# Performance work log

Measured on AMD Instinct MI355X. Metric: run time of the kernel, lower is better.

## Reference

```python
import jax, jax.numpy as jnp
import numpy as np

N_HEAD = 16

def _proj1x1(W, b, x):
    # kernel-size-1 Conv1d == channel-wise linear: x (B, C_in, T) -> (B, C_out, T)
    return jnp.einsum('oc,bct->bot', W, x) + b[None, :, None]

def setup_inputs() -> dict:
    key = jax.random.key(0)
    B, C, T = 2, 512, 2048
    ks = jax.random.split(key, 11)
    s = 0.02
    return {
        'q': jax.random.normal(ks[0], (B, C, T), jnp.float32),
        'k': jax.random.normal(ks[1], (B, C, T), jnp.float32),
        'v': jax.random.normal(ks[2], (B, C, T), jnp.float32),
        'mask': jnp.ones((B, 1, T), dtype=bool),
        'Wq': jax.random.normal(ks[3], (C, C), jnp.float32) * s,
        'bq': jax.random.normal(ks[4], (C,), jnp.float32) * s,
        'Wk': jax.random.normal(ks[5], (C, C), jnp.float32) * s,
        'bk': jax.random.normal(ks[6], (C,), jnp.float32) * s,
        'Wv': jax.random.normal(ks[7], (C, C), jnp.float32) * s,
        'bv': jax.random.normal(ks[8], (C,), jnp.float32) * s,
        'Wp': jax.random.normal(ks[9], (C, C), jnp.float32) * s,
        'bp': jax.random.normal(ks[10], (C,), jnp.float32) * s,
    }

def reference(q, k, v, mask, Wq, bq, Wk, bk, Wv, bv, Wp, bp):
    B, C, T = q.shape
    H = N_HEAD
    D = C // H
    scale = 1.0 / np.sqrt(D).astype(np.float32)
    # 1x1 conv projections, then split heads: (B,C,T) -> (B,H,T,D)
    qh = _proj1x1(Wq, bq, q).reshape(B, H, D, T).swapaxes(2, 3)
    kh = _proj1x1(Wk, bk, k).reshape(B, H, D, T).swapaxes(2, 3)
    vh = _proj1x1(Wv, bv, v).reshape(B, H, D, T).swapaxes(2, 3)
    # scores (B,H,Tq,Tk) with key-side mask
    att = jnp.einsum('bhqd,bhkd->bhqk', qh * scale, kh)
    att = jnp.where(mask[:, :, None, :], att, -jnp.inf)
    att = jax.nn.softmax(att, axis=-1)
    # value masking (as in original: v * mask before AV matmul)
    vm = vh * mask[:, :, :, None].astype(vh.dtype)
    out = jnp.einsum('bhqk,bhkd->bhqd', att, vm)
    out = out.swapaxes(2, 3).reshape(B, C, T)
    out = _proj1x1(Wp, bp, out) * mask.astype(out.dtype)
    return (out, mask)
```

## Files before the change

### kernel.cpp

```cpp
#include <hip/hip_runtime.h>

using u16 = unsigned short;
typedef float  f32x4 __attribute__((ext_vector_type(4)));
typedef __bf16 bf8_t __attribute__((ext_vector_type(8)));
typedef u16    u16x4 __attribute__((ext_vector_type(4)));
typedef unsigned int u32x2 __attribute__((ext_vector_type(2)));

#define NB 2
#define NH 16
#define NT 2048
#define ND 32
#define NC 512
#define QK_SCALE 0.17677669529663687f
#define LOG2E    1.4426950408889634f

__device__ __forceinline__ u16 f2bf(float f) {
  unsigned int u = __float_as_uint(f);
  u += 0x7fffu + ((u >> 16) & 1u);
  return (u16)(u >> 16);
}

__device__ __forceinline__ unsigned int cvt_pk_bf16(float a, float b) {
  unsigned int r;
  asm("v_cvt_pk_bf16_f32 %0, %1, %2" : "=v"(r) : "v"(a), "v"(b));
  return r;
}

__device__ __forceinline__ f32x4 mfma16(bf8_t a, bf8_t b, f32x4 c) {
  return __builtin_amdgcn_mfma_f32_16x16x32_bf16(a, b, c, 0, 0, 0);
}

__global__ __launch_bounds__(256) void convert_kernel(
    const float* __restrict__ Wq, const float* __restrict__ Wk,
    const float* __restrict__ Wv, const float* __restrict__ Wp,
    const void* __restrict__ mraw,
    u16* __restrict__ Wc, float* __restrict__ maskf, float* __restrict__ maskb,
    float* __restrict__ outtail) {
  int bid = blockIdx.x;
  if (bid < 1024) {
    int idx = (bid * 256 + (int)threadIdx.x) * 4;
    int m   = idx >> 18;
    int off = idx & 262143;
    const float* W = (m == 0) ? Wq : (m == 1) ? Wk : (m == 2) ? Wv : Wp;
    float s = (m == 0) ? (QK_SCALE * LOG2E) : 1.0f;
    f32x4 wv = *(const f32x4*)(W + off);
    u16x4 pk;
    #pragma unroll
    for (int r = 0; r < 4; ++r) pk[r] = f2bf(wv[r] * s);
    *(u16x4*)(Wc + (size_t)m * (NC * NC) + off) = pk;
  } else {
    unsigned int w0 = *(const unsigned int*)mraw;
    bool intlay = (w0 == 1u);
    #pragma unroll
    for (int kk = 0; kk < 16; ++kk) {
      int j = (int)threadIdx.x + kk * 256;
      float mv;
      if (intlay) mv = ((const int*)mraw)[j] ? 1.0f : 0.0f;
      else        mv = ((const unsigned char*)mraw)[j] ? 1.0f : 0.0f;
      maskf[j]   = mv;
      maskb[j]   = (mv - 1.0f) * 1e30f;
      outtail[j] = mv;
    }
  }
}

__global__ __launch_bounds__(256) void transpose_kernel(
    const float* __restrict__ q, const float* __restrict__ k,
    const float* __restrict__ v, u16* __restrict__ Xt) {
  __shared__ float tile[32][33];
  int z = blockIdx.z;
  int m = z >> 1, b = z & 1;
  const float* src = (m == 0) ? q : (m == 1) ? k : v;
  int t0 = blockIdx.x * 32, c0 = blockIdx.y * 32;
  int tx = threadIdx.x, ty = threadIdx.y;
  #pragma unroll
  for (int j = 0; j < 4; ++j)
    tile[ty + j * 8][tx] = src[(size_t)(b * NC + c0 + ty + j * 8) * NT + t0 + tx];
  __syncthreads();
  u16* dst = Xt + (size_t)m * (NB * NT * NC);
  #pragma unroll
  for (int j = 0; j < 4; ++j)
    dst[((size_t)b * NT + t0 + ty + j * 8) * NC + c0 + tx] = f2bf(tile[tx][ty + j * 8]);
}

__global__ __launch_bounds__(256) void proj_kernel(
    const u16* __restrict__ Wc, const u16* __restrict__ Xt,
    const float* __restrict__ bq, const float* __restrict__ bk, const float* __restrict__ bv,
    u16* __restrict__ Qw, u16* __restrict__ Kw, u16* __restrict__ Vw,
    const float* __restrict__ maskf) {
  int z = blockIdx.z;
  const u16* W = Wc + (size_t)z * (NC * NC);
  const float* bias = (z == 0) ? bq : (z == 1) ? bk : bv;
  int tid = threadIdx.x, wid = tid >> 6, lane = tid & 63;
  int lq = lane & 15, g = lane >> 4;
  int om0 = blockIdx.x * 64;
  int b   = blockIdx.y >> 4;
  int t0  = (blockIdx.y & 15) * 128 + wid * 32;
  const u16* Xb = Xt + (size_t)z * (NB * NT * NC) + (size_t)b * NT * NC;

  const f32x4 zero = {0.f, 0.f, 0.f, 0.f};
  f32x4 acc[4][2];
  #pragma unroll
  for (int mt = 0; mt < 4; ++mt)
    #pragma unroll
    for (int nt = 0; nt < 2; ++nt) acc[mt][nt] = zero;

  for (int ks = 0; ks < 16; ++ks) {
    bf8_t af[4], bfr[2];
    #pragma unroll
    for (int mt = 0; mt < 4; ++mt)
      af[mt] = *(const bf8_t*)(W + (size_t)(om0 + mt * 16 + lq) * NC + ks * 32 + 8 * g);
    #pragma unroll
    for (int nt = 0; nt < 2; ++nt)
      bfr[nt] = *(const bf8_t*)(Xb + (size_t)(t0 + nt * 16 + lq) * NC + ks * 32 + 8 * g);
    #pragma unroll
    for (int mt = 0; mt < 4; ++mt)
      #pragma unroll
      for (int nt = 0; nt < 2; ++nt)
        acc[mt][nt] = mfma16(af[mt], bfr[nt], acc[mt][nt]);
  }

  float sc = (z == 0) ? (QK_SCALE * LOG2E) : 1.0f;
  #pragma unroll
  for (int mt = 0; mt < 4; ++mt) {
    int ob = om0 + mt * 16 + 4 * g;
    float b4[4];
    #pragma unroll
    for (int r = 0; r < 4; ++r) b4[r] = bias[ob + r] * sc;
    #pragma unroll
    for (int nt = 0; nt < 2; ++nt) {
      int t = t0 + nt * 16 + lq;
      if (z < 2) {
        u16x4 pk;
        #pragma unroll
        for (int r = 0; r < 4; ++r) pk[r] = f2bf(acc[mt][nt][r] + b4[r]);
        u16* dst = (z == 0) ? Qw : Kw;
        *(u16x4*)(dst + ((size_t)(b * NH + (ob >> 5)) * NT + t) * ND + (ob & 31)) = pk;
      } else {
        float mv = maskf[b * NT + t];
        #pragma unroll
        for (int r = 0; r < 4; ++r)
          Vw[(size_t)(b * NC + ob + r) * NT + t] = f2bf((acc[mt][nt][r] + b4[r]) * mv);
      }
    }
  }
}

__global__ __launch_bounds__(256) void attn_kernel(
    const u16* __restrict__ Qw, const u16* __restrict__ Kw, const u16* __restrict__ Vw,
    u16* __restrict__ Ow, const float* __restrict__ maskb) {
  __shared__ u16 plds[4][32][128];
  int tid = threadIdx.x, wid = tid >> 6, lane = tid & 63;
  int lq = lane & 15, g = lane >> 4;
  int bh = blockIdx.y, b = bh >> 4, h = bh & 15;
  int q0 = blockIdx.x * 128 + wid * 32;
  const u16* Qb = Qw + (size_t)bh * NT * ND;
  const u16* Kb = Kw + (size_t)bh * NT * ND;
  const u16* Vb = Vw + (size_t)(b * NC + h * ND) * NT;
  const float* mbp = maskb + b * NT;
  char* pbase = (char*)&plds[wid][0][0];

  bf8_t ones;
  #pragma unroll
  for (int j = 0; j < 8; ++j) ones[j] = (__bf16)1.0f;

  bf8_t qf[2];
  #pragma unroll
  for (int c = 0; c < 2; ++c)
    qf[c] = *(const bf8_t*)(Qb + (size_t)(q0 + c * 16 + lq) * ND + 8 * g);

  const f32x4 zero = {0.f, 0.f, 0.f, 0.f};
  f32x4 acc[3][2];
  #pragma unroll
  for (int dt = 0; dt < 3; ++dt)
    #pragma unroll
    for (int c = 0; c < 2; ++c) acc[dt][c] = zero;
  float mrun[2] = {0.f, 0.f};

  for (int kt = 0; kt < 16; ++kt) {
    int tkb = kt * 128;
    f32x4 st[8][2];
    #pragma unroll
    for (int rt = 0; rt < 8; ++rt) {
      f32x4 bias = *(const f32x4*)(mbp + tkb + rt * 16 + 4 * g);
      bf8_t kf = *(const bf8_t*)(Kb + (size_t)(tkb + rt * 16 + lq) * ND + 8 * g);
      st[rt][0] = mfma16(kf, qf[0], bias);
      st[rt][1] = mfma16(kf, qf[1], bias);
    }
    bf8_t vf[2][4];
    #pragma unroll
    for (int dt = 0; dt < 2; ++dt)
      #pragma unroll
      for (int kk = 0; kk < 4; ++kk)
        vf[dt][kk] = *(const bf8_t*)(Vb + (size_t)(dt * 16 + lq) * NT + tkb + kk * 32 + 8 * g);

    #pragma unroll
    for (int c = 0; c < 2; ++c) {
      float tm = -1e30f;
      #pragma unroll
      for (int rt = 0; rt < 8; ++rt) {
        tm = fmaxf(fmaxf(st[rt][c][0], st[rt][c][1]), tm);
        tm = fmaxf(fmaxf(st[rt][c][2], st[rt][c][3]), tm);
      }
      tm = fmaxf(tm, __shfl_xor(tm, 16));
      tm = fmaxf(tm, __shfl_xor(tm, 32));
      if (__any(tm > mrun[c] + 8.0f)) {
        float mnew = fmaxf(mrun[c], tm);
        float al = __builtin_amdgcn_exp2f(mrun[c] - mnew);
        mrun[c] = mnew;
        acc[0][c] *= al; acc[1][c] *= al; acc[2][c] *= al;
      }
      float nm = -mrun[c];
      int row = c * 16 + lq;
      #pragma unroll
      for (int rt = 0; rt < 8; ++rt) {
        float p0 = __builtin_amdgcn_exp2f(st[rt][c][0] + nm);
        float p1 = __builtin_amdgcn_exp2f(st[rt][c][1] + nm);
        float p2 = __builtin_amdgcn_exp2f(st[rt][c][2] + nm);
        float p3 = __builtin_amdgcn_exp2f(st[rt][c][3] + nm);
        u32x2 w;
        w[0] = cvt_pk_bf16(p0, p1);
        w[1] = cvt_pk_bf16(p2, p3);
        *(u32x2*)(pbase + row * 256 + ((rt * 32 + 8 * g) ^ ((row & 7) << 4))) = w;
      }
    }
    #pragma unroll
    for (int kk = 0; kk < 4; ++kk) {
      bf8_t pf[2];
      #pragma unroll
      for (int c = 0; c < 2; ++c) {
        int row = c * 16 + lq;
        pf[c] = *(const bf8_t*)(pbase + row * 256 + ((kk * 64 + 16 * g) ^ ((row & 7) << 4)));
      }
      #pragma unroll
      for (int c = 0; c < 2; ++c) {
        acc[0][c] = mfma16(vf[0][kk], pf[c], acc[0][c]);
        acc[1][c] = mfma16(vf[1][kk], pf[c], acc[1][c]);
        acc[2][c] = mfma16(ones,      pf[c], acc[2][c]);
      }
    }
  }
  #pragma unroll
  for (int c = 0; c < 2; ++c) {
    float inv = 1.0f / acc[2][c][0];
    int t = q0 + c * 16 + lq;
    #pragma unroll
    for (int dt = 0; dt < 2; ++dt) {
      u32x2 o;
      o[0] = cvt_pk_bf16(acc[dt][c][0] * inv, acc[dt][c][1] * inv);
      o[1] = cvt_pk_bf16(acc[dt][c][2] * inv, acc[dt][c][3] * inv);
      *(u32x2*)(Ow + ((size_t)bh * NT + t) * ND + dt * 16 + 4 * g) = o;
    }
  }
}

__global__ __launch_bounds__(256) void outproj_kernel(
    const u16* __restrict__ Wc, const u16* __restrict__ Ow,
    const float* __restrict__ bp, float* __restrict__ out,
    const float* __restrict__ maskf) {
  const u16* W = Wc + (size_t)3 * NC * NC;
  int tid = threadIdx.x, wid = tid >> 6, lane = tid & 63;
  int lq = lane & 15, g = lane >> 4;
  int om0 = blockIdx.x * 64;
  int b   = blockIdx.y >> 4;
  int t0  = (blockIdx.y & 15) * 128 + wid * 32;
  const u16* Ob = Ow + (size_t)b * NH * NT * ND;

  const f32x4 zero = {0.f, 0.f, 0.f, 0.f};
  f32x4 acc[4][2];
  #pragma unroll
  for (int mt = 0; mt < 4; ++mt)
    #pragma unroll
    for (int nt = 0; nt < 2; ++nt) acc[mt][nt] = zero;

  for (int ks = 0; ks < 16; ++ks) {
    bf8_t af[4], bfr[2];
    #pragma unroll
    for (int mt = 0; mt < 4; ++mt)
      af[mt] = *(const bf8_t*)(W + (size_t)(om0 + mt * 16 + lq) * NC + ks * 32 + 8 * g);
    #pragma unroll
    for (int nt = 0; nt < 2; ++nt)
      bfr[nt] = *(const bf8_t*)(Ob + ((size_t)ks * NT + t0 + nt * 16 + lq) * ND + 8 * g);
    #pragma unroll
    for (int mt = 0; mt < 4; ++mt)
      #pragma unroll
      for (int nt = 0; nt < 2; ++nt)
        acc[mt][nt] = mfma16(af[mt], bfr[nt], acc[mt][nt]);
  }
  #pragma unroll
  for (int mt = 0; mt < 4; ++mt) {
    int ob = om0 + mt * 16 + 4 * g;
    float b4[4];
    #pragma unroll
    for (int r = 0; r < 4; ++r) b4[r] = bp[ob + r];
    #pragma unroll
    for (int nt = 0; nt < 2; ++nt) {
      int t = t0 + nt * 16 + lq;
      float mv = maskf[b * NT + t];
      #pragma unroll
      for (int r = 0; r < 4; ++r)
        out[(size_t)(b * NC + ob + r) * NT + t] = (acc[mt][nt][r] + b4[r]) * mv;
    }
  }
}

extern "C" void kernel_launch(void* const* d_in, const int* in_sizes, int n_in,
                              void* d_out, int out_size, void* d_ws, size_t ws_size,
                              hipStream_t stream) {
  const float* q  = (const float*)d_in[0];
  const float* k  = (const float*)d_in[1];
  const float* v  = (const float*)d_in[2];
  const void*  mr = d_in[3];
  const float* Wq = (const float*)d_in[4];
  const float* bq = (const float*)d_in[5];
  const float* Wk = (const float*)d_in[6];
  const float* bk = (const float*)d_in[7];
  const float* Wv = (const float*)d_in[8];
  const float* bv = (const float*)d_in[9];
  const float* Wp = (const float*)d_in[10];
  const float* bp = (const float*)d_in[11];
  float* out = (float*)d_out;

  u16* Wc = (u16*)d_ws;
  u16* Xt = Wc + (size_t)4 * NC * NC;
  u16* Qw = Xt + (size_t)3 * NB * NT * NC;
  u16* Kw = Qw + (size_t)NB * NT * NC;
  u16* Vw = Kw + (size_t)NB * NT * NC;
  u16* Ow = Vw + (size_t)NB * NT * NC;
  float* maskf   = (float*)(Ow + (size_t)NB * NT * NC);
  float* maskb   = maskf + (size_t)NB * NT;
  float* outtail = out + (size_t)NB * NC * NT;

  convert_kernel<<<1025, 256, 0, stream>>>(Wq, Wk, Wv, Wp, mr, Wc, maskf, maskb, outtail);
  transpose_kernel<<<dim3(NT / 32, NC / 32, 6), dim3(32, 8), 0, stream>>>(q, k, v, Xt);
  proj_kernel<<<dim3(8, 32, 3), 256, 0, stream>>>(Wc, Xt, bq, bk, bv, Qw, Kw, Vw, maskf);
  attn_kernel<<<dim3(16, 32), 256, 0, stream>>>(Qw, Kw, Vw, Ow, maskb);
  outproj_kernel<<<dim3(8, 32), 256, 0, stream>>>(Wc, Ow, bp, out, maskf);
}
```

Before: 203.9 us.

## Shrink per-block tiles to raise grid size and add register prefetch in GEMMs

Halves the output tile per block in the projection, attention and output-projection kernels, doubling or quadrupling the number of blocks so more CUs are busy on this small problem. The GEMM loops now software-prefetch the next k-slice into registers while issuing MFMAs. Attention handles 16 query rows per wave instead of 32 and lowers the lazy-rescale threshold. The trade is less data reuse per wave, more redundant K/V and weight loads, and more launch overhead from extra blocks.

```diff
diff --git a/kernel.cpp b/kernel.cpp
--- a/kernel.cpp
+++ b/kernel.cpp
@@ -83,7 +83,7 @@
     dst[((size_t)b * NT + t0 + ty + j * 8) * NC + c0 + tx] = f2bf(tile[tx][ty + j * 8]);
 }
 
-__global__ __launch_bounds__(256) void proj_kernel(
+__global__ __launch_bounds__(256, 4) void proj_kernel(
     const u16* __restrict__ Wc, const u16* __restrict__ Xt,
     const float* __restrict__ bq, const float* __restrict__ bk, const float* __restrict__ bv,
     u16* __restrict__ Qw, u16* __restrict__ Kw, u16* __restrict__ Vw,
@@ -93,36 +93,36 @@
   const float* bias = (z == 0) ? bq : (z == 1) ? bk : bv;
   int tid = threadIdx.x, wid = tid >> 6, lane = tid & 63;
   int lq = lane & 15, g = lane >> 4;
-  int om0 = blockIdx.x * 64;
+  int om0 = blockIdx.x * 32;
   int b   = blockIdx.y >> 4;
   int t0  = (blockIdx.y & 15) * 128 + wid * 32;
   const u16* Xb = Xt + (size_t)z * (NB * NT * NC) + (size_t)b * NT * NC;
 
+  const u16* Wr0 = W  + (size_t)(om0 + lq) * NC + 8 * g;
+  const u16* Wr1 = W  + (size_t)(om0 + 16 + lq) * NC + 8 * g;
+  const u16* Xr0 = Xb + (size_t)(t0 + lq) * NC + 8 * g;
+  const u16* Xr1 = Xb + (size_t)(t0 + 16 + lq) * NC + 8 * g;
+
   const f32x4 zero = {0.f, 0.f, 0.f, 0.f};
-  f32x4 acc[4][2];
-  #pragma unroll
-  for (int mt = 0; mt < 4; ++mt)
-    #pragma unroll
-    for (int nt = 0; nt < 2; ++nt) acc[mt][nt] = zero;
-
+  f32x4 acc[2][2];
+  acc[0][0] = zero; acc[0][1] = zero; acc[1][0] = zero; acc[1][1] = zero;
+
+  bf8_t a0 = *(const bf8_t*)Wr0, a1 = *(const bf8_t*)Wr1;
+  bf8_t x0 = *(const bf8_t*)Xr0, x1 = *(const bf8_t*)Xr1;
   for (int ks = 0; ks < 16; ++ks) {
-    bf8_t af[4], bfr[2];
-    #pragma unroll
-    for (int mt = 0; mt < 4; ++mt)
-      af[mt] = *(const bf8_t*)(W + (size_t)(om0 + mt * 16 + lq) * NC + ks * 32 + 8 * g);
-    #pragma unroll
-    for (int nt = 0; nt < 2; ++nt)
-      bfr[nt] = *(const bf8_t*)(Xb + (size_t)(t0 + nt * 16 + lq) * NC + ks * 32 + 8 * g);
-    #pragma unroll
-    for (int mt = 0; mt < 4; ++mt)
-      #pragma unroll
-      for (int nt = 0; nt < 2; ++nt)
-        acc[mt][nt] = mfma16(af[mt], bfr[nt], acc[mt][nt]);
+    int kn = (ks < 15 ? ks + 1 : ks) * 32;
+    bf8_t an0 = *(const bf8_t*)(Wr0 + kn), an1 = *(const bf8_t*)(Wr1 + kn);
+    bf8_t xn0 = *(const bf8_t*)(Xr0 + kn), xn1 = *(const bf8_t*)(Xr1 + kn);
+    acc[0][0] = mfma16(a0, x0, acc[0][0]);
+    acc[0][1] = mfma16(a0, x1, acc[0][1]);
+    acc[1][0] = mfma16(a1, x0, acc[1][0]);
+    acc[1][1] = mfma16(a1, x1, acc[1][1]);
+    a0 = an0; a1 = an1; x0 = xn0; x1 = xn1;
   }
 
   float sc = (z == 0) ? (QK_SCALE * LOG2E) : 1.0f;
   #pragma unroll
-  for (int mt = 0; mt < 4; ++mt) {
+  for (int mt = 0; mt < 2; ++mt) {
     int ob = om0 + mt * 16 + 4 * g;
     float b4[4];
     #pragma unroll
@@ -146,14 +146,14 @@
   }
 }
 
-__global__ __launch_bounds__(256) void attn_kernel(
+__global__ __launch_bounds__(256, 4) void attn_kernel(
     const u16* __restrict__ Qw, const u16* __restrict__ Kw, const u16* __restrict__ Vw,
     u16* __restrict__ Ow, const float* __restrict__ maskb) {
-  __shared__ u16 plds[4][32][128];
+  __shared__ u16 plds[4][16][128];
   int tid = threadIdx.x, wid = tid >> 6, lane = tid & 63;
   int lq = lane & 15, g = lane >> 4;
   int bh = blockIdx.y, b = bh >> 4, h = bh & 15;
-  int q0 = blockIdx.x * 128 + wid * 32;
+  int q0 = blockIdx.x * 64 + wid * 16;
   const u16* Qb = Qw + (size_t)bh * NT * ND;
   const u16* Kb = Kw + (size_t)bh * NT * ND;
   const u16* Vb = Vw + (size_t)(b * NC + h * ND) * NT;
@@ -164,28 +164,21 @@
   #pragma unroll
   for (int j = 0; j < 8; ++j) ones[j] = (__bf16)1.0f;
 
-  bf8_t qf[2];
-  #pragma unroll
-  for (int c = 0; c < 2; ++c)
-    qf[c] = *(const bf8_t*)(Qb + (size_t)(q0 + c * 16 + lq) * ND + 8 * g);
+  bf8_t qf = *(const bf8_t*)(Qb + (size_t)(q0 + lq) * ND + 8 * g);
 
   const f32x4 zero = {0.f, 0.f, 0.f, 0.f};
-  f32x4 acc[3][2];
-  #pragma unroll
-  for (int dt = 0; dt < 3; ++dt)
-    #pragma unroll
-    for (int c = 0; c < 2; ++c) acc[dt][c] = zero;
-  float mrun[2] = {0.f, 0.f};
+  f32x4 acc[3];
+  acc[0] = zero; acc[1] = zero; acc[2] = zero;
+  float mrun = 0.f;
 
   for (int kt = 0; kt < 16; ++kt) {
     int tkb = kt * 128;
-    f32x4 st[8][2];
+    f32x4 st[8];
     #pragma unroll
     for (int rt = 0; rt < 8; ++rt) {
       f32x4 bias = *(const f32x4*)(mbp + tkb + rt * 16 + 4 * g);
       bf8_t kf = *(const bf8_t*)(Kb + (size_t)(tkb + rt * 16 + lq) * ND + 8 * g);
-      st[rt][0] = mfma16(kf, qf[0], bias);
-      st[rt][1] = mfma16(kf, qf[1], bias);
+      st[rt] = mfma16(kf, qf, bias);
     }
     bf8_t vf[2][4];
     #pragma unroll
@@ -194,113 +187,89 @@
       for (int kk = 0; kk < 4; ++kk)
         vf[dt][kk] = *(const bf8_t*)(Vb + (size_t)(dt * 16 + lq) * NT + tkb + kk * 32 + 8 * g);
 
-    #pragma unroll
-    for (int c = 0; c < 2; ++c) {
-      float tm = -1e30f;
-      #pragma unroll
-      for (int rt = 0; rt < 8; ++rt) {
-        tm = fmaxf(fmaxf(st[rt][c][0], st[rt][c][1]), tm);
-        tm = fmaxf(fmaxf(st[rt][c][2], st[rt][c][3]), tm);
-      }
-      tm = fmaxf(tm, __shfl_xor(tm, 16));
-      tm = fmaxf(tm, __shfl_xor(tm, 32));
-      if (__any(tm > mrun[c] + 8.0f)) {
-        float mnew = fmaxf(mrun[c], tm);
-        float al = __builtin_amdgcn_exp2f(mrun[c] - mnew);
-        mrun[c] = mnew;
-        acc[0][c] *= al; acc[1][c] *= al; acc[2][c] *= al;
-      }
-      float nm = -mrun[c];
-      int row = c * 16 + lq;
-      #pragma unroll
-      for (int rt = 0; rt < 8; ++rt) {
-        float p0 = __builtin_amdgcn_exp2f(st[rt][c][0] + nm);
-        float p1 = __builtin_amdgcn_exp2f(st[rt][c][1] + nm);
-        float p2 = __builtin_amdgcn_exp2f(st[rt][c][2] + nm);
-        float p3 = __builtin_amdgcn_exp2f(st[rt][c][3] + nm);
-        u32x2 w;
-        w[0] = cvt_pk_bf16(p0, p1);
-        w[1] = cvt_pk_bf16(p2, p3);
-        *(u32x2*)(pbase + row * 256 + ((rt * 32 + 8 * g) ^ ((row & 7) << 4))) = w;
-      }
+    float tm = -1e30f;
+    #pragma unroll
+    for (int rt = 0; rt < 8; ++rt) {
+      tm = fmaxf(fmaxf(st[rt][0], st[rt][1]), tm);
+      tm = fmaxf(fmaxf(st[rt][2], st[rt][3]), tm);
+    }
+    tm = fmaxf(tm, __shfl_xor(tm, 16));
+    tm = fmaxf(tm, __shfl_xor(tm, 32));
+    if (__any(tm > mrun + 2.0f)) {
+      float mnew = fmaxf(mrun, tm);
+      float al = __builtin_amdgcn_exp2f(mrun - mnew);
+      mrun = mnew;
+      acc[0] *= al; acc[1] *= al; acc[2] *= al;
+    }
+    float nm = -mrun;
+    #pragma unroll
+    for (int rt = 0; rt < 8; ++rt) {
+      float p0 = __builtin_amdgcn_exp2f(st[rt][0] + nm);
+      float p1 = __builtin_amdgcn_exp2f(st[rt][1] + nm);
+      float p2 = __builtin_amdgcn_exp2f(st[rt][2] + nm);
+      float p3 = __builtin_amdgcn_exp2f(st[rt][3] + nm);
+      u32x2 w;
+      w[0] = cvt_pk_bf16(p0, p1);
+      w[1] = cvt_pk_bf16(p2, p3);
+      *(u32x2*)(pbase + lq * 256 + ((rt * 32 + 8 * g) ^ ((lq & 7) << 4))) = w;
     }
     #pragma unroll
     for (int kk = 0; kk < 4; ++kk) {
-      bf8_t pf[2];
-      #pragma unroll
-      for (int c = 0; c < 2; ++c) {
-        int row = c * 16 + lq;
-        pf[c] = *(const bf8_t*)(pbase + row * 256 + ((kk * 64 + 16 * g) ^ ((row & 7) << 4)));
-      }
-      #pragma unroll
-      for (int c = 0; c < 2; ++c) {
-        acc[0][c] = mfma16(vf[0][kk], pf[c], acc[0][c]);
-        acc[1][c] = mfma16(vf[1][kk], pf[c], acc[1][c]);
-        acc[2][c] = mfma16(ones,      pf[c], acc[2][c]);
-      }
-    }
-  }
-  #pragma unroll
-  for (int c = 0; c < 2; ++c) {
-    float inv = 1.0f / acc[2][c][0];
-    int t = q0 + c * 16 + lq;
-    #pragma unroll
-    for (int dt = 0; dt < 2; ++dt) {
-      u32x2 o;
-      o[0] = cvt_pk_bf16(acc[dt][c][0] * inv, acc[dt][c][1] * inv);
-      o[1] = cvt_pk_bf16(acc[dt][c][2] * inv, acc[dt][c][3] * inv);
-      *(u32x2*)(Ow + ((size_t)bh * NT + t) * ND + dt * 16 + 4 * g) = o;
-    }
-  }
-}
-
-__global__ __launch_bounds__(256) void outproj_kernel(
+      bf8_t pf = *(const bf8_t*)(pbase + lq * 256 + ((kk * 64 + 16 * g) ^ ((lq & 7) << 4)));
+      acc[0] = mfma16(vf[0][kk], pf, acc[0]);
+      acc[1] = mfma16(vf[1][kk], pf, acc[1]);
+      acc[2] = mfma16(ones,      pf, acc[2]);
+    }
+  }
+  float inv = 1.0f / acc[2][0];
+  int t = q0 + lq;
+  #pragma unroll
+  for (int dt = 0; dt < 2; ++dt) {
+    u32x2 o;
+    o[0] = cvt_pk_bf16(acc[dt][0] * inv, acc[dt][1] * inv);
+    o[1] = cvt_pk_bf16(acc[dt][2] * inv, acc[dt][3] * inv);
+    *(u32x2*)(Ow + ((size_t)bh * NT + t) * ND + dt * 16 + 4 * g) = o;
+  }
+}
+
+__global__ __launch_bounds__(256, 4) void outproj_kernel(
     const u16* __restrict__ Wc, const u16* __restrict__ Ow,
     const float* __restrict__ bp, float* __restrict__ out,
     const float* __restrict__ maskf) {
   const u16* W = Wc + (size_t)3 * NC * NC;
   int tid = threadIdx.x, wid = tid >> 6, lane = tid & 63;
   int lq = lane & 15, g = lane >> 4;
-  int om0 = blockIdx.x * 64;
-  int b   = blockIdx.y >> 4;
-  int t0  = (blockIdx.y & 15) * 128 + wid * 32;
+  int om0 = blockIdx.x * 32;
+  int b   = blockIdx.y >> 5;
+  int t0  = (blockIdx.y & 31) * 64 + wid * 16;
   const u16* Ob = Ow + (size_t)b * NH * NT * ND;
 
+  const u16* Wr0 = W + (size_t)(om0 + lq) * NC + 8 * g;
+  const u16* Wr1 = W + (size_t)(om0 + 16 + lq) * NC + 8 * g;
+
   const f32x4 zero = {0.f, 0.f, 0.f, 0.f};
-  f32x4 acc[4][2];
-  #pragma unroll
-  for (int mt = 0; mt < 4; ++mt)
-    #pragma unroll
-    for (int nt = 0; nt < 2; ++nt) acc[mt][nt] = zero;
-
+  f32x4 acc0 = zero, acc1 = zero;
+
+  bf8_t a0 = *(const bf8_t*)Wr0, a1 = *(const bf8_t*)Wr1;
+  bf8_t x0 = *(const bf8_t*)(Ob + (size_t)(t0 + lq) * ND + 8 * g);
   for (int ks = 0; ks < 16; ++ks) {
-    bf8_t af[4], bfr[2];
-    #pragma unroll
-    for (int mt = 0; mt < 4; ++mt)
-      af[mt] = *(const bf8_t*)(W + (size_t)(om0 + mt * 16 + lq) * NC + ks * 32 + 8 * g);
-    #pragma unroll
-    for (int nt = 0; nt < 2; ++nt)
-      bfr[nt] = *(const bf8_t*)(Ob + ((size_t)ks * NT + t0 + nt * 16 + lq) * ND + 8 * g);
-    #pragma unroll
-    for (int mt = 0; mt < 4; ++mt)
-      #pragma unroll
-      for (int nt = 0; nt < 2; ++nt)
-        acc[mt][nt] = mfma16(af[mt], bfr[nt], acc[mt][nt]);
-  }
-  #pragma unroll
-  for (int mt = 0; mt < 4; ++mt) {
+    int kn = (ks < 15) ? ks + 1 : ks;
+    bf8_t an0 = *(const bf8_t*)(Wr0 + kn * 32);
+    bf8_t an1 = *(const bf8_t*)(Wr1 + kn * 32);
+    bf8_t xn0 = *(const bf8_t*)(Ob + ((size_t)kn * NT + t0 + lq) * ND + 8 * g);
+    acc0 = mfma16(a0, x0, acc0);
+    acc1 = mfma16(a1, x0, acc1);
+    a0 = an0; a1 = an1; x0 = xn0;
+  }
+  int t = t0 + lq;
+  float mv = maskf[b * NT + t];
+  #pragma unroll
+  for (int mt = 0; mt < 2; ++mt) {
     int ob = om0 + mt * 16 + 4 * g;
-    float b4[4];
-    #pragma unroll
-    for (int r = 0; r < 4; ++r) b4[r] = bp[ob + r];
-    #pragma unroll
-    for (int nt = 0; nt < 2; ++nt) {
-      int t = t0 + nt * 16 + lq;
-      float mv = maskf[b * NT + t];
-      #pragma unroll
-      for (int r = 0; r < 4; ++r)
-        out[(size_t)(b * NC + ob + r) * NT + t] = (acc[mt][nt][r] + b4[r]) * mv;
-    }
+    const f32x4& a = mt ? acc1 : acc0;
+    #pragma unroll
+    for (int r = 0; r < 4; ++r)
+      out[(size_t)(b * NC + ob + r) * NT + t] = (a[r] + bp[ob + r]) * mv;
   }
 }
 
@@ -333,7 +302,7 @@
 
   convert_kernel<<<1025, 256, 0, stream>>>(Wq, Wk, Wv, Wp, mr, Wc, maskf, maskb, outtail);
   transpose_kernel<<<dim3(NT / 32, NC / 32, 6), dim3(32, 8), 0, stream>>>(q, k, v, Xt);
-  proj_kernel<<<dim3(8, 32, 3), 256, 0, stream>>>(Wc, Xt, bq, bk, bv, Qw, Kw, Vw, maskf);
-  attn_kernel<<<dim3(16, 32), 256, 0, stream>>>(Qw, Kw, Vw, Ow, maskb);
-  outproj_kernel<<<dim3(8, 32), 256, 0, stream>>>(Wc, Ow, bp, out, maskf);
-}
+  proj_kernel<<<dim3(16, 32, 3), 256, 0, stream>>>(Wc, Xt, bq, bk, bv, Qw, Kw, Vw, maskf);
+  attn_kernel<<<dim3(32, 32), 256, 0, stream>>>(Qw, Kw, Vw, Ow, maskb);
+  outproj_kernel<<<dim3(16, 64), 256, 0, stream>>>(Wc, Ow, bp, out, maskf);
+}
```

New measurement: 265.7 us. 30.3% more time.

## Split attention over key halves and merge partials inside output projection

Applied to the files above, without the earlier changes.

The attention kernel now splits the key sequence into two halves across a new grid dimension, which doubles the block count to fill more compute units. Each half writes unnormalized fp32 partial outputs plus its running max and sum. The output projection kernel merges the two partials with log-sum-exp rescaling before its MFMA, and uses smaller tiles for more blocks. The cost is extra fp32 partial traffic to global memory and merge arithmetic in the projection. The rescale threshold is also lowered from 8 to 2, and launch bounds are added.

```diff
diff --git a/kernel.cpp b/kernel.cpp
--- a/kernel.cpp
+++ b/kernel.cpp
@@ -146,13 +146,14 @@
   }
 }
 
-__global__ __launch_bounds__(256) void attn_kernel(
+__global__ __launch_bounds__(256, 4) void attn_kernel(
     const u16* __restrict__ Qw, const u16* __restrict__ Kw, const u16* __restrict__ Vw,
-    u16* __restrict__ Ow, const float* __restrict__ maskb) {
+    float* __restrict__ Op, float* __restrict__ ml, const float* __restrict__ maskb) {
   __shared__ u16 plds[4][32][128];
   int tid = threadIdx.x, wid = tid >> 6, lane = tid & 63;
   int lq = lane & 15, g = lane >> 4;
   int bh = blockIdx.y, b = bh >> 4, h = bh & 15;
+  int z  = blockIdx.z;
   int q0 = blockIdx.x * 128 + wid * 32;
   const u16* Qb = Qw + (size_t)bh * NT * ND;
   const u16* Kb = Kw + (size_t)bh * NT * ND;
@@ -177,7 +178,7 @@
     for (int c = 0; c < 2; ++c) acc[dt][c] = zero;
   float mrun[2] = {0.f, 0.f};
 
-  for (int kt = 0; kt < 16; ++kt) {
+  for (int kt = z * 8; kt < z * 8 + 8; ++kt) {
     int tkb = kt * 128;
     f32x4 st[8][2];
     #pragma unroll
@@ -204,7 +205,7 @@
       }
       tm = fmaxf(tm, __shfl_xor(tm, 16));
       tm = fmaxf(tm, __shfl_xor(tm, 32));
-      if (__any(tm > mrun[c] + 8.0f)) {
+      if (__any(tm > mrun[c] + 2.0f)) {
         float mnew = fmaxf(mrun[c], tm);
         float al = __builtin_amdgcn_exp2f(mrun[c] - mnew);
         mrun[c] = mnew;
@@ -240,67 +241,74 @@
       }
     }
   }
+  size_t pofs = (size_t)z * NB * NH * NT * ND;
+  size_t mofs = (size_t)z * NB * NH * NT;
   #pragma unroll
   for (int c = 0; c < 2; ++c) {
-    float inv = 1.0f / acc[2][c][0];
     int t = q0 + c * 16 + lq;
-    #pragma unroll
-    for (int dt = 0; dt < 2; ++dt) {
-      u32x2 o;
-      o[0] = cvt_pk_bf16(acc[dt][c][0] * inv, acc[dt][c][1] * inv);
-      o[1] = cvt_pk_bf16(acc[dt][c][2] * inv, acc[dt][c][3] * inv);
-      *(u32x2*)(Ow + ((size_t)bh * NT + t) * ND + dt * 16 + 4 * g) = o;
-    }
-  }
-}
-
-__global__ __launch_bounds__(256) void outproj_kernel(
-    const u16* __restrict__ Wc, const u16* __restrict__ Ow,
+    if (g == 0) {
+      float2 mlv; mlv.x = mrun[c]; mlv.y = acc[2][c][0];
+      *(float2*)(ml + (mofs + (size_t)bh * NT + t) * 2) = mlv;
+    }
+    #pragma unroll
+    for (int dt = 0; dt < 2; ++dt)
+      *(f32x4*)(Op + pofs + ((size_t)bh * NT + t) * ND + dt * 16 + 4 * g) = acc[dt][c];
+  }
+}
+
+__global__ __launch_bounds__(256, 4) void outproj_kernel(
+    const u16* __restrict__ Wc, const float* __restrict__ Op,
+    const float* __restrict__ ml,
     const float* __restrict__ bp, float* __restrict__ out,
     const float* __restrict__ maskf) {
   const u16* W = Wc + (size_t)3 * NC * NC;
   int tid = threadIdx.x, wid = tid >> 6, lane = tid & 63;
   int lq = lane & 15, g = lane >> 4;
-  int om0 = blockIdx.x * 64;
-  int b   = blockIdx.y >> 4;
-  int t0  = (blockIdx.y & 15) * 128 + wid * 32;
-  const u16* Ob = Ow + (size_t)b * NH * NT * ND;
+  int om0 = blockIdx.x * 32;
+  int b   = blockIdx.y >> 5;
+  int t0  = (blockIdx.y & 31) * 64 + wid * 16;
+  int t   = t0 + lq;
+
+  const u16* Wr0 = W + (size_t)(om0 + lq) * NC + 8 * g;
+  const u16* Wr1 = W + (size_t)(om0 + 16 + lq) * NC + 8 * g;
+  const size_t PS = (size_t)NB * NH * NT * ND;
+  const size_t MS = (size_t)NB * NH * NT;
 
   const f32x4 zero = {0.f, 0.f, 0.f, 0.f};
-  f32x4 acc[4][2];
-  #pragma unroll
-  for (int mt = 0; mt < 4; ++mt)
-    #pragma unroll
-    for (int nt = 0; nt < 2; ++nt) acc[mt][nt] = zero;
+  f32x4 acc0 = zero, acc1 = zero;
 
   for (int ks = 0; ks < 16; ++ks) {
-    bf8_t af[4], bfr[2];
-    #pragma unroll
-    for (int mt = 0; mt < 4; ++mt)
-      af[mt] = *(const bf8_t*)(W + (size_t)(om0 + mt * 16 + lq) * NC + ks * 32 + 8 * g);
-    #pragma unroll
-    for (int nt = 0; nt < 2; ++nt)
-      bfr[nt] = *(const bf8_t*)(Ob + ((size_t)ks * NT + t0 + nt * 16 + lq) * ND + 8 * g);
-    #pragma unroll
-    for (int mt = 0; mt < 4; ++mt)
-      #pragma unroll
-      for (int nt = 0; nt < 2; ++nt)
-        acc[mt][nt] = mfma16(af[mt], bfr[nt], acc[mt][nt]);
-  }
-  #pragma unroll
-  for (int mt = 0; mt < 4; ++mt) {
+    bf8_t a0 = *(const bf8_t*)(Wr0 + ks * 32);
+    bf8_t a1 = *(const bf8_t*)(Wr1 + ks * 32);
+    size_t qb = (size_t)(b * NH + ks) * NT + t;
+    float2 v1 = *(const float2*)(ml + qb * 2);
+    float2 v2 = *(const float2*)(ml + (MS + qb) * 2);
+    size_t ob = qb * ND + 8 * g;
+    f32x4 o1a = *(const f32x4*)(Op + ob);
+    f32x4 o1b = *(const f32x4*)(Op + ob + 4);
+    f32x4 o2a = *(const f32x4*)(Op + PS + ob);
+    f32x4 o2b = *(const f32x4*)(Op + PS + ob + 4);
+    float m  = fmaxf(v1.x, v2.x);
+    float e1 = __builtin_amdgcn_exp2f(v1.x - m);
+    float e2 = __builtin_amdgcn_exp2f(v2.x - m);
+    float inv = 1.0f / (v1.y * e1 + v2.y * e2);
+    float c1 = e1 * inv, c2 = e2 * inv;
+    union { bf8_t v; unsigned int u[4]; } xf;
+    xf.u[0] = cvt_pk_bf16(o1a[0] * c1 + o2a[0] * c2, o1a[1] * c1 + o2a[1] * c2);
+    xf.u[1] = cvt_pk_bf16(o1a[2] * c1 + o2a[2] * c2, o1a[3] * c1 + o2a[3] * c2);
+    xf.u[2] = cvt_pk_bf16(o1b[0] * c1 + o2b[0] * c2, o1b[1] * c1 + o2b[1] * c2);
+    xf.u[3] = cvt_pk_bf16(o1b[2] * c1 + o2b[2] * c2, o1b[3] * c1 + o2b[3] * c2);
+    acc0 = mfma16(a0, xf.v, acc0);
+    acc1 = mfma16(a1, xf.v, acc1);
+  }
+  float mv = maskf[b * NT + t];
+  #pragma unroll
+  for (int mt = 0; mt < 2; ++mt) {
     int ob = om0 + mt * 16 + 4 * g;
-    float b4[4];
-    #pragma unroll
-    for (int r = 0; r < 4; ++r) b4[r] = bp[ob + r];
-    #pragma unroll
-    for (int nt = 0; nt < 2; ++nt) {
-      int t = t0 + nt * 16 + lq;
-      float mv = maskf[b * NT + t];
-      #pragma unroll
-      for (int r = 0; r < 4; ++r)
-        out[(size_t)(b * NC + ob + r) * NT + t] = (acc[mt][nt][r] + b4[r]) * mv;
-    }
+    const f32x4& a = mt ? acc1 : acc0;
+    #pragma unroll
+    for (int r = 0; r < 4; ++r)
+      out[(size_t)(b * NC + ob + r) * NT + t] = (a[r] + bp[ob + r]) * mv;
   }
 }
 
@@ -326,14 +334,15 @@
   u16* Qw = Xt + (size_t)3 * NB * NT * NC;
   u16* Kw = Qw + (size_t)NB * NT * NC;
   u16* Vw = Kw + (size_t)NB * NT * NC;
-  u16* Ow = Vw + (size_t)NB * NT * NC;
-  float* maskf   = (float*)(Ow + (size_t)NB * NT * NC);
-  float* maskb   = maskf + (size_t)NB * NT;
+  float* Op    = (float*)(Vw + (size_t)NB * NT * NC);
+  float* ml    = Op + (size_t)2 * NB * NH * NT * ND;
+  float* maskf = ml + (size_t)2 * NB * NH * NT * 2;
+  float* maskb = maskf + (size_t)NB * NT;
   float* outtail = out + (size_t)NB * NC * NT;
 
   convert_kernel<<<1025, 256, 0, stream>>>(Wq, Wk, Wv, Wp, mr, Wc, maskf, maskb, outtail);
   transpose_kernel<<<dim3(NT / 32, NC / 32, 6), dim3(32, 8), 0, stream>>>(q, k, v, Xt);
   proj_kernel<<<dim3(8, 32, 3), 256, 0, stream>>>(Wc, Xt, bq, bk, bv, Qw, Kw, Vw, maskf);
-  attn_kernel<<<dim3(16, 32), 256, 0, stream>>>(Qw, Kw, Vw, Ow, maskb);
-  outproj_kernel<<<dim3(8, 32), 256, 0, stream>>>(Wc, Ow, bp, out, maskf);
-}
+  attn_kernel<<<dim3(16, 32, 2), 256, 0, stream>>>(Qw, Kw, Vw, Op, ml, maskb);
+  outproj_kernel<<<dim3(16, 64), 256, 0, stream>>>(Wc, Op, ml, bp, out, maskf);
+}
```

New measurement: 271.1 us. 1.33x slower.

## Split attention KV range across wave pairs and fuse prep kernels

Applied to the files above, without the earlier changes.

The attention kernel now gives each block 64 queries and splits the 16 KV tiles between two wave pairs. The partial accumulators, running maxima and sums are merged through shared memory at the end, and the grid doubles to 1024 blocks for better occupancy and latency hiding. The weight/mask conversion and the input transpose are merged into one launch to remove a kernel launch. The rescale threshold drops from 8 to 2, and launch bounds request 4 blocks per SM. The costs are extra syncs, an LDS merge step and duplicated Q loads.

```diff
diff --git a/kernel.cpp b/kernel.cpp
--- a/kernel.cpp
+++ b/kernel.cpp
@@ -30,15 +30,20 @@
   return __builtin_amdgcn_mfma_f32_16x16x32_bf16(a, b, c, 0, 0, 0);
 }
 
-__global__ __launch_bounds__(256) void convert_kernel(
+__global__ __launch_bounds__(256) void prep_kernel(
+    const float* __restrict__ q, const float* __restrict__ k,
+    const float* __restrict__ v, u16* __restrict__ Xt,
     const float* __restrict__ Wq, const float* __restrict__ Wk,
     const float* __restrict__ Wv, const float* __restrict__ Wp,
     const void* __restrict__ mraw,
     u16* __restrict__ Wc, float* __restrict__ maskf, float* __restrict__ maskb,
     float* __restrict__ outtail) {
-  int bid = blockIdx.x;
-  if (bid < 1024) {
-    int idx = (bid * 256 + (int)threadIdx.x) * 4;
+  int z = blockIdx.z;
+  int tx = threadIdx.x, ty = threadIdx.y;
+  if (z == 6) {
+    int bid = blockIdx.y * 64 + blockIdx.x;
+    int tid = ty * 32 + tx;
+    int idx = (bid * 256 + tid) * 4;
     int m   = idx >> 18;
     int off = idx & 262143;
     const float* W = (m == 0) ? Wq : (m == 1) ? Wk : (m == 2) ? Wv : Wp;
@@ -48,31 +53,26 @@
     #pragma unroll
     for (int r = 0; r < 4; ++r) pk[r] = f2bf(wv[r] * s);
     *(u16x4*)(Wc + (size_t)m * (NC * NC) + off) = pk;
-  } else {
-    unsigned int w0 = *(const unsigned int*)mraw;
-    bool intlay = (w0 == 1u);
-    #pragma unroll
-    for (int kk = 0; kk < 16; ++kk) {
-      int j = (int)threadIdx.x + kk * 256;
-      float mv;
-      if (intlay) mv = ((const int*)mraw)[j] ? 1.0f : 0.0f;
-      else        mv = ((const unsigned char*)mraw)[j] ? 1.0f : 0.0f;
-      maskf[j]   = mv;
-      maskb[j]   = (mv - 1.0f) * 1e30f;
-      outtail[j] = mv;
-    }
-  }
-}
-
-__global__ __launch_bounds__(256) void transpose_kernel(
-    const float* __restrict__ q, const float* __restrict__ k,
-    const float* __restrict__ v, u16* __restrict__ Xt) {
+    if (bid == 0) {
+      unsigned int w0 = *(const unsigned int*)mraw;
+      bool intlay = (w0 == 1u);
+      #pragma unroll
+      for (int kk = 0; kk < 16; ++kk) {
+        int j = tid + kk * 256;
+        float mv;
+        if (intlay) mv = ((const int*)mraw)[j] ? 1.0f : 0.0f;
+        else        mv = ((const unsigned char*)mraw)[j] ? 1.0f : 0.0f;
+        maskf[j]   = mv;
+        maskb[j]   = (mv - 1.0f) * 1e30f;
+        outtail[j] = mv;
+      }
+    }
+    return;
+  }
   __shared__ float tile[32][33];
-  int z = blockIdx.z;
   int m = z >> 1, b = z & 1;
   const float* src = (m == 0) ? q : (m == 1) ? k : v;
   int t0 = blockIdx.x * 32, c0 = blockIdx.y * 32;
-  int tx = threadIdx.x, ty = threadIdx.y;
   #pragma unroll
   for (int j = 0; j < 4; ++j)
     tile[ty + j * 8][tx] = src[(size_t)(b * NC + c0 + ty + j * 8) * NT + t0 + tx];
@@ -146,14 +146,15 @@
   }
 }
 
-__global__ __launch_bounds__(256) void attn_kernel(
+__global__ __launch_bounds__(256, 4) void attn_kernel(
     const u16* __restrict__ Qw, const u16* __restrict__ Kw, const u16* __restrict__ Vw,
     u16* __restrict__ Ow, const float* __restrict__ maskb) {
   __shared__ u16 plds[4][32][128];
   int tid = threadIdx.x, wid = tid >> 6, lane = tid & 63;
   int lq = lane & 15, g = lane >> 4;
   int bh = blockIdx.y, b = bh >> 4, h = bh & 15;
-  int q0 = blockIdx.x * 128 + wid * 32;
+  int kvz = wid >> 1;
+  int q0  = blockIdx.x * 64 + (wid & 1) * 32;
   const u16* Qb = Qw + (size_t)bh * NT * ND;
   const u16* Kb = Kw + (size_t)bh * NT * ND;
   const u16* Vb = Vw + (size_t)(b * NC + h * ND) * NT;
@@ -177,7 +178,7 @@
     for (int c = 0; c < 2; ++c) acc[dt][c] = zero;
   float mrun[2] = {0.f, 0.f};
 
-  for (int kt = 0; kt < 16; ++kt) {
+  for (int kt = kvz * 8; kt < kvz * 8 + 8; ++kt) {
     int tkb = kt * 128;
     f32x4 st[8][2];
     #pragma unroll
@@ -204,7 +205,7 @@
       }
       tm = fmaxf(tm, __shfl_xor(tm, 16));
       tm = fmaxf(tm, __shfl_xor(tm, 32));
-      if (__any(tm > mrun[c] + 8.0f)) {
+      if (__any(tm > mrun[c] + 2.0f)) {
         float mnew = fmaxf(mrun[c], tm);
         float al = __builtin_amdgcn_exp2f(mrun[c] - mnew);
         mrun[c] = mnew;
@@ -240,16 +241,49 @@
       }
     }
   }
-  #pragma unroll
-  for (int c = 0; c < 2; ++c) {
-    float inv = 1.0f / acc[2][c][0];
-    int t = q0 + c * 16 + lq;
-    #pragma unroll
-    for (int dt = 0; dt < 2; ++dt) {
-      u32x2 o;
-      o[0] = cvt_pk_bf16(acc[dt][c][0] * inv, acc[dt][c][1] * inv);
-      o[1] = cvt_pk_bf16(acc[dt][c][2] * inv, acc[dt][c][3] * inv);
-      *(u32x2*)(Ow + ((size_t)bh * NT + t) * ND + dt * 16 + 4 * g) = o;
+
+  __syncthreads();
+  float* cb = (float*)plds;
+  if (wid >= 2) {
+    int p = wid - 2;
+    char* cbO = (char*)(cb + p * 1024);
+    float* cbML = cb + 2048 + p * 64;
+    #pragma unroll
+    for (int c = 0; c < 2; ++c) {
+      int row = c * 16 + lq;
+      #pragma unroll
+      for (int dt = 0; dt < 2; ++dt)
+        *(f32x4*)(cbO + row * 128 + ((dt * 64 + g * 16) ^ ((lq & 7) << 4))) = acc[dt][c];
+      if (g == 0) {
+        float2 mlv; mlv.x = mrun[c]; mlv.y = acc[2][c][0];
+        *(float2*)(cbML + row * 2) = mlv;
+      }
+    }
+  }
+  __syncthreads();
+  if (wid < 2) {
+    char* cbO = (char*)(cb + wid * 1024);
+    float* cbML = cb + 2048 + wid * 64;
+    #pragma unroll
+    for (int c = 0; c < 2; ++c) {
+      int row = c * 16 + lq;
+      float2 ml2 = *(const float2*)(cbML + row * 2);
+      float m  = fmaxf(mrun[c], ml2.x);
+      float e1 = __builtin_amdgcn_exp2f(mrun[c] - m);
+      float e2 = __builtin_amdgcn_exp2f(ml2.x - m);
+      float inv = 1.0f / (acc[2][c][0] * e1 + ml2.y * e2);
+      float c1 = e1 * inv, c2 = e2 * inv;
+      int t = q0 + row;
+      #pragma unroll
+      for (int dt = 0; dt < 2; ++dt) {
+        f32x4 o2 = *(const f32x4*)(cbO + row * 128 + ((dt * 64 + g * 16) ^ ((lq & 7) << 4)));
+        u32x2 o;
+        o[0] = cvt_pk_bf16(acc[dt][c][0] * c1 + o2[0] * c2,
+                           acc[dt][c][1] * c1 + o2[1] * c2);
+        o[1] = cvt_pk_bf16(acc[dt][c][2] * c1 + o2[2] * c2,
+                           acc[dt][c][3] * c1 + o2[3] * c2);
+        *(u32x2*)(Ow + ((size_t)bh * NT + t) * ND + dt * 16 + 4 * g) = o;
+      }
     }
   }
 }
@@ -331,9 +365,9 @@
   float* maskb   = maskf + (size_t)NB * NT;
   float* outtail = out + (size_t)NB * NC * NT;
 
-  convert_kernel<<<1025, 256, 0, stream>>>(Wq, Wk, Wv, Wp, mr, Wc, maskf, maskb, outtail);
-  transpose_kernel<<<dim3(NT / 32, NC / 32, 6), dim3(32, 8), 0, stream>>>(q, k, v, Xt);
+  prep_kernel<<<dim3(64, 16, 7), dim3(32, 8), 0, stream>>>(
+      q, k, v, Xt, Wq, Wk, Wv, Wp, mr, Wc, maskf, maskb, outtail);
   proj_kernel<<<dim3(8, 32, 3), 256, 0, stream>>>(Wc, Xt, bq, bk, bv, Qw, Kw, Vw, maskf);
-  attn_kernel<<<dim3(16, 32), 256, 0, stream>>>(Qw, Kw, Vw, Ow, maskb);
+  attn_kernel<<<dim3(32, 32), 256, 0, stream>>>(Qw, Kw, Vw, Ow, maskb);
   outproj_kernel<<<dim3(8, 32), 256, 0, stream>>>(Wc, Ow, bp, out, maskf);
 }
```

Result: slower. 263.8 us (+29.4%).
